# Performance work log

Measured on AMD Instinct MI355X. Metric: run time of the kernel, lower is better.

## Reference

```python
import jax, jax.numpy as jnp
import numpy as np
import math
from jax import lax

HID, H, K = 1024, 8, 4
D = HID // H
B, T = 2, 2048
CLAMP_MAX = 0.999995
LN_EPS = 1e-5

def _logit(x):
    x = min(max(x, 1e-06), 1 - 1e-06)
    return math.log(x / (1 - x))

def setup_inputs() -> dict:
    key = jax.random.key(0)
    ks = jax.random.split(key, 8)
    def xavier(k, fan_in, fan_out):
        s = math.sqrt(2.0 / (fan_in + fan_out))
        return jax.random.normal(k, (fan_in, fan_out), jnp.float32) * s
    x = jax.random.normal(ks[0], (B, T, HID), jnp.float32)
    mask = jnp.ones((B, T), jnp.float32)
    Wq = xavier(ks[1], HID, HID)
    Wk = xavier(ks[2], HID, HID)
    Wv = xavier(ks[3], HID, HID)
    Wb = xavier(ks[4], HID, H)
    bb = jnp.full((H,), _logit(0.99), jnp.float32)
    Wm = xavier(ks[5], HID, H * K)
    bm = jnp.zeros((H * K,), jnp.float32)
    Wo = xavier(ks[6], HID, HID)
    bo = jnp.zeros((HID,), jnp.float32)
    base = np.array([_logit(math.exp(-1.0 / t)) for t in [16.0, 64.0, 256.0, 1024.0]], np.float32)
    base_logit = jnp.asarray(np.tile(base[None, :], (H, 1)))  # (H, K)
    ln_g = jnp.ones((HID,), jnp.float32)
    ln_b = jnp.zeros((HID,), jnp.float32)
    return dict(x=x, mask=mask, Wq=Wq, Wk=Wk, Wv=Wv, Wb=Wb, bb=bb, Wm=Wm, bm=bm,
                Wo=Wo, bo=bo, base_logit=base_logit, ln_g=ln_g, ln_b=ln_b)

def _delta_scan(q, k, v, beta, mix, mask, base_logit):
    # q,k,v: (B,T,H,D); beta: (B,T,H); mix: (B,T,H,K); mask: (B,T)
    b, t = q.shape[0], q.shape[1]
    base_r = jax.nn.sigmoid(base_logit)  # (H,K)
    state0 = jnp.zeros((b, H, K, D, D), jnp.float32)

    def step(state, inp):
        q_t, k_t, v_t, b_t, mix_t, m_t = inp
        valid = (m_t > 0)[:, None, None, None, None]            # (B,1,1,1,1)
        r_eff = jnp.clip(b_t[:, :, None] * base_r[None], 0.0, CLAMP_MAX)  # (B,H,K)
        outer = jnp.einsum('bhd,bhe->bhde', k_t, v_t)[:, :, None]          # (B,H,1,D,D)
        new_state = jnp.where(valid, state * r_eff[..., None, None] + outer, state)
        o_scales = jnp.einsum('bhd,bhkde->bhke', q_t, new_state)           # (B,H,K,D)
        w = jax.nn.softmax(mix_t, axis=-1)                                  # (B,H,K)
        o_t = jnp.sum(w[..., None] * o_scales, axis=2)                      # (B,H,D)
        o_t = o_t * (m_t > 0)[:, None, None].astype(o_t.dtype)
        return new_state, o_t

    xs = (jnp.moveaxis(q, 1, 0), jnp.moveaxis(k, 1, 0), jnp.moveaxis(v, 1, 0),
          jnp.moveaxis(beta, 1, 0), jnp.moveaxis(mix, 1, 0), jnp.moveaxis(mask, 1, 0))
    _, outs = lax.scan(step, state0, xs)       # (T,B,H,D)
    return jnp.moveaxis(outs, 0, 1)            # (B,T,H,D)

def reference(x, mask, Wq, Wk, Wv, Wb, bb, Wm, bm, Wo, bo, base_logit, ln_g, ln_b):
    b, t, _ = x.shape
    def elu1(z):
        return jax.nn.elu(z) + 1.0
    q = elu1((x @ Wq).reshape(b, t, H, D))
    k = elu1((x @ Wk).reshape(b, t, H, D))
    v = (x @ Wv).reshape(b, t, H, D)
    beta = jax.nn.sigmoid(x @ Wb + bb)               # (B,T,H)
    mix = (x @ Wm + bm).reshape(b, t, H, K)          # (B,T,H,K)
    head_out = _delta_scan(q, k, v, beta, mix, mask, base_logit)  # (B,T,H,D)
    out = head_out.reshape(b, t, HID) @ Wo + bo
    y = x + out                                       # residual (dropout in eval mode)
    mu = jnp.mean(y, axis=-1, keepdims=True)
    var = jnp.mean((y - mu) ** 2, axis=-1, keepdims=True)
    return (y - mu) * lax.rsqrt(var + LN_EPS) * ln_g + ln_b
```

## Files before the change

### kernel.cpp

```cpp
#include <hip/hip_runtime.h>
#include <hip/hip_bf16.h>
#include <math.h>

#define TSEQ 2048
#define NHID 1024

typedef float f32x4 __attribute__((ext_vector_type(4)));
typedef __bf16 bf16x8 __attribute__((ext_vector_type(8)));

static __device__ __forceinline__ unsigned short f2bf(float f) {
  unsigned u = __float_as_uint(f);
  u += 0x7fffu + ((u >> 16) & 1u);
  return (unsigned short)(u >> 16);
}
static __device__ __forceinline__ float bf2f(unsigned short h) {
  return __uint_as_float(((unsigned)h) << 16);
}

#define GLDS16(g, l) __builtin_amdgcn_global_load_lds( \
    (const __attribute__((address_space(1))) unsigned int*)(g), \
    (__attribute__((address_space(3))) unsigned int*)(l), 16, 0, 0)

__global__ __launch_bounds__(256) void transpose_all_kernel(
    const float* __restrict__ Wq, const float* __restrict__ Wk,
    const float* __restrict__ Wv, const float* __restrict__ Wo,
    unsigned short* __restrict__ Wqkvt, unsigned short* __restrict__ Wto) {
  __shared__ float tile[32][33];
  const float* W;
  unsigned short* Wt;
  int m = blockIdx.z;
  if (m == 0)      { W = Wq; Wt = Wqkvt; }
  else if (m == 1) { W = Wk; Wt = Wqkvt + 1024 * 1024; }
  else if (m == 2) { W = Wv; Wt = Wqkvt + 2 * 1024 * 1024; }
  else             { W = Wo; Wt = Wto; }
  int bx = blockIdx.x * 32;
  int by = blockIdx.y * 32;
  int tx = threadIdx.x, ty = threadIdx.y;
#pragma unroll
  for (int i = 0; i < 32; i += 8)
    tile[ty + i][tx] = W[(size_t)(by + ty + i) * NHID + bx + tx];
  __syncthreads();
#pragma unroll
  for (int i = 0; i < 32; i += 8)
    Wt[(size_t)(bx + ty + i) * NHID + by + tx] = f2bf(tile[tx][ty + i]);
}

template <int MODE>
__global__ __launch_bounds__(256) void gemm_pipe_kernel(
    const unsigned short* __restrict__ A, const unsigned short* __restrict__ Bt,
    unsigned short* __restrict__ Oq, unsigned short* __restrict__ Ok,
    unsigned short* __restrict__ Ov, float* __restrict__ Cf,
    const float* __restrict__ bias, const float* __restrict__ res) {
  __shared__ __align__(16) unsigned short As[3 * 4096];
  __shared__ __align__(16) unsigned short Bs[3 * 4096];
  const int tid = threadIdx.x;
  const int lane = tid & 63;
  const int wave = tid >> 6;
  const int wr = wave >> 1, wc = wave & 1;
  const int rowBase = blockIdx.y * 128;
  const int colBase = blockIdx.x * 128;

  const int c0 = wave * 128 + lane;
  const int c1 = c0 + 64;
  const int r0 = c0 >> 2, kc0 = (c0 & 3) ^ ((r0 >> 1) & 3);
  const int r1 = c1 >> 2, kc1 = (c1 & 3) ^ ((r1 >> 1) & 3);
  const unsigned short* gA0 = A + (size_t)(rowBase + r0) * 1024 + kc0 * 8;
  const unsigned short* gA1 = A + (size_t)(rowBase + r1) * 1024 + kc1 * 8;
  const unsigned short* gB0 = Bt + (size_t)(colBase + r0) * 1024 + kc0 * 8;
  const unsigned short* gB1 = Bt + (size_t)(colBase + r1) * 1024 + kc1 * 8;
  const int wofs = wave * 1024;

  const int kq = lane >> 4;
  const int r16 = lane & 15;

  f32x4 acc[4][4] = {};

#define STAGE(buf, k0)                                       \
  do {                                                       \
    GLDS16(gA0 + (k0), &As[(buf) * 4096 + wofs]);            \
    GLDS16(gA1 + (k0), &As[(buf) * 4096 + wofs + 512]);      \
    GLDS16(gB0 + (k0), &Bs[(buf) * 4096 + wofs]);            \
    GLDS16(gB1 + (k0), &Bs[(buf) * 4096 + wofs + 512]);      \
  } while (0)

  STAGE(0, 0);
  STAGE(1, 32);
  int cur = 0, stg = 2;
  for (int t = 0; t < 32; ++t) {
    if (t < 30) {
      STAGE(stg, (t + 2) * 32);
      asm volatile("s_waitcnt vmcnt(8)" ::: "memory");
    } else if (t == 30) {
      asm volatile("s_waitcnt vmcnt(4)" ::: "memory");
    } else {
      asm volatile("s_waitcnt vmcnt(0)" ::: "memory");
    }
    __builtin_amdgcn_s_barrier();
    asm volatile("" ::: "memory");
    const unsigned short* Ac = &As[cur * 4096];
    const unsigned short* Bc = &Bs[cur * 4096];
    bf16x8 af[4], bfr[4];
#pragma unroll
    for (int m = 0; m < 4; ++m) {
      int row = wr * 64 + m * 16 + r16;
      af[m] = *(const bf16x8*)(Ac + row * 32 + (kq ^ ((row >> 1) & 3)) * 8);
      int colr = wc * 64 + m * 16 + r16;
      bfr[m] = *(const bf16x8*)(Bc + colr * 32 + (kq ^ ((colr >> 1) & 3)) * 8);
    }
    __builtin_amdgcn_s_setprio(1);
#pragma unroll
    for (int m = 0; m < 4; ++m)
#pragma unroll
      for (int n = 0; n < 4; ++n)
        acc[m][n] = __builtin_amdgcn_mfma_f32_16x16x32_bf16(af[m], bfr[n], acc[m][n], 0, 0, 0);
    __builtin_amdgcn_s_setprio(0);
    asm volatile("" ::: "memory");
    __builtin_amdgcn_s_barrier();
    asm volatile("" ::: "memory");
    cur = (cur == 2) ? 0 : cur + 1;
    stg = (stg == 2) ? 0 : stg + 1;
  }
#undef STAGE

  const int r4 = (lane >> 4) * 4;
  if (MODE == 1) {
#pragma unroll
    for (int m = 0; m < 4; ++m)
#pragma unroll
      for (int n = 0; n < 4; ++n) {
        int col = colBase + wc * 64 + n * 16 + r16;
#pragma unroll
        for (int j = 0; j < 4; ++j) {
          int row = rowBase + wr * 64 + m * 16 + r4 + j;
          Cf[(size_t)row * 1024 + col] = acc[m][n][j] + bias[col] + res[(size_t)row * 1024 + col];
        }
      }
  } else {
    unsigned short* outp;
    int cb;
    bool elu;
    if (colBase < 1024)      { outp = Oq; cb = colBase;        elu = true;  }
    else if (colBase < 2048) { outp = Ok; cb = colBase - 1024; elu = true;  }
    else                     { outp = Ov; cb = colBase - 2048; elu = false; }
#pragma unroll
    for (int m = 0; m < 4; ++m)
#pragma unroll
      for (int n = 0; n < 4; ++n) {
        int col = cb + wc * 64 + n * 16 + r16;
#pragma unroll
        for (int j = 0; j < 4; ++j) {
          int row = rowBase + wr * 64 + m * 16 + r4 + j;
          float v = acc[m][n][j];
          if (elu) v = (v > 0.f) ? (v + 1.f) : expf(v);
          outp[(size_t)row * 1024 + col] = f2bf(v);
        }
      }
  }
}

__global__ __launch_bounds__(256) void pack_wbm_kernel(const float* __restrict__ Wb,
    const float* __restrict__ Wm, float* __restrict__ Wt) {
  int id = blockIdx.x * 256 + threadIdx.x;
  if (id >= 40960) return;
  int o = id >> 10, i = id & 1023;
  Wt[id] = (o < 8) ? Wb[i * 8 + o] : Wm[i * 32 + (o - 8)];
}

__global__ __launch_bounds__(256) void rw2_kernel(const float* __restrict__ x,
    const float* __restrict__ Wt, const float* __restrict__ bb,
    const float* __restrict__ bm, const float* __restrict__ base_logit,
    float* __restrict__ R, float* __restrict__ Wsm,
    unsigned short* __restrict__ Xb) {
  int row = blockIdx.x;
  __shared__ float xs[1024];
  __shared__ float outs[40];
  int tid = threadIdx.x;
  float4 xv = *(const float4*)(x + (size_t)row * 1024 + tid * 4);
  *(float4*)(xs + tid * 4) = xv;
  ushort4 xo;
  xo.x = f2bf(xv.x); xo.y = f2bf(xv.y); xo.z = f2bf(xv.z); xo.w = f2bf(xv.w);
  *(ushort4*)(Xb + (size_t)row * 1024 + tid * 4) = xo;
  __syncthreads();
  int wave = tid >> 6, lane = tid & 63;
  for (int o = wave; o < 40; o += 4) {
    const float* wr = Wt + o * 1024;
    float sum = 0.f;
#pragma unroll
    for (int it = 0; it < 16; ++it) {
      int i = it * 64 + lane;
      sum += xs[i] * wr[i];
    }
#pragma unroll
    for (int off = 32; off > 0; off >>= 1) sum += __shfl_down(sum, off);
    if (lane == 0) outs[o] = sum;
  }
  __syncthreads();
  if (tid < 32) {
    int h = tid >> 2;
    float beta = 1.f / (1.f + expf(-(outs[h] + bb[h])));
    float br = 1.f / (1.f + expf(-base_logit[tid]));
    float r = fminf(fmaxf(beta * br, 0.f), 0.999995f);
    float mval = outs[8 + tid] + bm[tid];
    float mx = fmaxf(mval, __shfl_xor(mval, 1));
    mx = fmaxf(mx, __shfl_xor(mx, 2));
    float ex = expf(mval - mx);
    float ssum = ex + __shfl_xor(ex, 1);
    ssum += __shfl_xor(ssum, 2);
    R[(size_t)row * 32 + tid] = r;
    Wsm[(size_t)row * 32 + tid] = ex / ssum;
  }
}

__global__ __launch_bounds__(256) void decay2_kernel(const float* __restrict__ R,
    const float* __restrict__ Wsm, const float* __restrict__ mask,
    float* __restrict__ WA, float* __restrict__ IA, float* __restrict__ DU,
    float* __restrict__ AC) {
  int wave = threadIdx.x >> 6, lane = threadIdx.x & 63;
  int id = blockIdx.x * 4 + wave;
  int c = id & 15, k = (id >> 4) & 3, bh = id >> 6;
  int b = bh >> 3, h = bh & 7;
  int row0 = b * TSEQ + c * 128 + 2 * lane;
  float m0 = mask[row0], m1 = mask[row0 + 1];
  size_t i0 = (size_t)row0 * 32 + h * 4 + k;
  float rr0 = (m0 > 0.f) ? R[i0] : 1.f;
  float rr1 = (m1 > 0.f) ? R[i0 + 32] : 1.f;
  float incl = rr0 * rr1;
#pragma unroll
  for (int off = 1; off < 64; off <<= 1) {
    float o = __shfl_up(incl, off);
    if (lane >= off) incl *= o;
  }
  float excl = __shfl_up(incl, 1);
  if (lane == 0) excl = 1.f;
  float a0 = fmaxf(excl * rr0, 1e-25f);
  float a1 = fmaxf(a0 * rr1, 1e-25f);
  float aC = __shfl(a1, 63);
  if (lane == 63) AC[(bh * 16 + c) * 4 + k] = a1;
  bool v0 = m0 > 0.f, v1 = m1 > 0.f;
  float w0 = Wsm[i0], w1 = Wsm[i0 + 32];
  int dub = ((bh * 16 + c) * 4 + k) * 128 + 2 * lane;
  WA[i0] = v0 ? w0 * a0 : 0.f;
  WA[i0 + 32] = v1 ? w1 * a1 : 0.f;
  IA[i0] = v0 ? 1.f / a0 : 0.f;
  IA[i0 + 32] = v1 ? 1.f / a1 : 0.f;
  DU[dub] = v0 ? aC / a0 : 0.f;
  DU[dub + 1] = v1 ? aC / a1 : 0.f;
}

__global__ __launch_bounds__(512) void chunkA_kernel(
    const unsigned short* __restrict__ Qb, const unsigned short* __restrict__ Kb,
    const unsigned short* __restrict__ Vb,
    const float* __restrict__ WA, const float* __restrict__ IA,
    const float* __restrict__ DU,
    float* __restrict__ Olocal, unsigned short* __restrict__ UT) {
  __shared__ __align__(16) char KTl[32768];
  __shared__ __align__(16) char VTl[32768];
  __shared__ __align__(16) char Pl[32768];
  __shared__ __align__(16) float WAl[128][4];
  __shared__ __align__(16) float IAl[128][4];
  __shared__ float DUl[4][128];

  int wg = blockIdx.x;
  int bh = wg >> 4, c = wg & 15;
  int b = bh >> 3, h = bh & 7;
  int t0 = c * 128;
  int tid = threadIdx.x;
  int lane = tid & 63, wave = tid >> 6;
  int wbase = wave * 16;
  int l15 = lane & 15, lq = lane >> 4;

  const size_t qkvbase = ((size_t)b * TSEQ + t0) * 1024 + h * 128;

  for (int it = 0; it < 4; ++it) {
    int ci = tid + it * 512;
    int t = ci >> 4, s = ci & 15;
    bf16x8 kv = *(const bf16x8*)(Kb + qkvbase + (size_t)t * 1024 + s * 8);
    bf16x8 vv = *(const bf16x8*)(Vb + qkvbase + (size_t)t * 1024 + s * 8);
#pragma unroll
    for (int e = 0; e < 8; ++e) {
      int d = s * 8 + e;
      int off = d * 256 + (((t >> 3) ^ (d & 7)) << 4) + (t & 7) * 2;
      *(unsigned short*)(KTl + off) = f2bf((float)kv[e]);
      *(unsigned short*)(VTl + off) = f2bf((float)vv[e]);
    }
  }
  {
    int t = tid >> 2, k = tid & 3;
    size_t idx = ((size_t)b * TSEQ + t0 + t) * 32 + h * 4 + k;
    WAl[t][k] = WA[idx];
    IAl[t][k] = IA[idx];
    int k2 = tid >> 7, j = tid & 127;
    DUl[k2][j] = DU[((bh * 16 + c) * 4 + k2) * 128 + j];
  }
  __syncthreads();

  bf16x8 qf[4];
#pragma unroll
  for (int ds = 0; ds < 4; ++ds)
    qf[ds] = *(const bf16x8*)(Qb + qkvbase + (size_t)(wbase + l15) * 1024 + ds * 32 + lq * 8);
  f32x4 accP[8];
#pragma unroll
  for (int jf = 0; jf < 8; ++jf) {
    f32x4 a = {};
#pragma unroll
    for (int ds = 0; ds < 4; ++ds) {
      bf16x8 kfrag = *(const bf16x8*)(Kb + qkvbase + (size_t)(jf * 16 + l15) * 1024 + ds * 32 + lq * 8);
      a = __builtin_amdgcn_mfma_f32_16x16x32_bf16(qf[ds], kfrag, a, 0, 0, 0);
    }
    accP[jf] = a;
  }

  float4 wa4[4];
#pragma unroll
  for (int jj = 0; jj < 4; ++jj)
    wa4[jj] = *(const float4*)&WAl[wbase + lq * 4 + jj][0];
#pragma unroll
  for (int jf = 0; jf < 8; ++jf) {
    float4 ia4 = *(const float4*)&IAl[jf * 16 + l15][0];
#pragma unroll
    for (int jj = 0; jj < 4; ++jj) {
      int tl = wbase + lq * 4 + jj;
      int jl = jf * 16 + l15;
      float m = 0.f;
      if (jl <= tl)
        m = wa4[jj].x * ia4.x + wa4[jj].y * ia4.y + wa4[jj].z * ia4.z + wa4[jj].w * ia4.w;
      float pv = accP[jf][jj] * m;
      int off = tl * 256 + (((jl >> 3) ^ (tl & 7)) << 4) + (jl & 7) * 2;
      *(unsigned short*)(Pl + off) = f2bf(pv);
    }
  }

  bf16x8 pf[4];
#pragma unroll
  for (int js = 0; js < 4; ++js) {
    int tl = wbase + l15;
    int slot = js * 4 + lq;
    pf[js] = *(const bf16x8*)(Pl + tl * 256 + ((slot ^ (tl & 7)) << 4));
  }
#pragma unroll
  for (int dvf = 0; dvf < 8; ++dvf) {
    f32x4 a = {};
    int dv = dvf * 16 + l15;
#pragma unroll
    for (int js = 0; js < 4; ++js) {
      int slot = js * 4 + lq;
      bf16x8 vfrag = *(const bf16x8*)(VTl + dv * 256 + ((slot ^ (dv & 7)) << 4));
      a = __builtin_amdgcn_mfma_f32_16x16x32_bf16(pf[js], vfrag, a, 0, 0, 0);
    }
#pragma unroll
    for (int jj = 0; jj < 4; ++jj) {
      int tl = wbase + lq * 4 + jj;
      Olocal[((size_t)b * TSEQ + t0 + tl) * 1024 + h * 128 + dv] = a[jj];
    }
  }

  if (c < 15) {
#pragma unroll 1
    for (int k = 0; k < 4; ++k) {
      f32x4 accU[8] = {};
#pragma unroll 1
      for (int js = 0; js < 4; ++js) {
        int dvr = wbase + l15;
        int slot = js * 4 + lq;
        bf16x8 af = *(const bf16x8*)(VTl + dvr * 256 + ((slot ^ (dvr & 7)) << 4));
        int j0 = js * 32 + lq * 8;
        bf16x8 afs;
#pragma unroll
        for (int e = 0; e < 8; ++e)
          afs[e] = (__bf16)((float)af[e] * DUl[k][j0 + e]);
#pragma unroll
        for (int dkf = 0; dkf < 8; ++dkf) {
          int dk = dkf * 16 + l15;
          bf16x8 kf = *(const bf16x8*)(KTl + dk * 256 + ((slot ^ (dk & 7)) << 4));
          accU[dkf] = __builtin_amdgcn_mfma_f32_16x16x32_bf16(afs, kf, accU[dkf], 0, 0, 0);
        }
      }
      size_t ub = (((size_t)bh * 16 + c) * 4 + k) * 16384;
#pragma unroll
      for (int dkf = 0; dkf < 8; ++dkf) {
        int dk = dkf * 16 + l15;
#pragma unroll
        for (int jj = 0; jj < 4; ++jj) {
          int dvr = wbase + lq * 4 + jj;
          UT[ub + (size_t)dvr * 128 + dk] = f2bf(accU[dkf][jj]);
        }
      }
    }
  }
}

__global__ __launch_bounds__(256) void chainB_kernel(const unsigned short* __restrict__ UT,
    const float* __restrict__ AC, unsigned short* __restrict__ S0T) {
  int id = blockIdx.x * 256 + threadIdx.x;
  int dk = id & 127;
  int dv = (id >> 7) & 127;
  int k = (id >> 14) & 3;
  int bh = id >> 16;
  size_t elem = (size_t)dv * 128 + dk;
  float S = 0.f;
#pragma unroll 1
  for (int c = 0; c < 15; ++c) {
    size_t ub = (((size_t)bh * 16 + c) * 4 + k) * 16384;
    float u = bf2f(UT[ub + elem]);
    float aC = AC[(bh * 16 + c) * 4 + k];
    S = aC * S + u;
    size_t sb = (((size_t)bh * 16 + (c + 1)) * 4 + k) * 16384;
    S0T[sb + elem] = f2bf(S);
  }
}

__global__ __launch_bounds__(512) void chunkC_kernel(const unsigned short* __restrict__ Qb,
    const unsigned short* __restrict__ S0T, const float* __restrict__ WA,
    const float* __restrict__ Olocal, unsigned short* __restrict__ Ob) {
  __shared__ __align__(16) char Sl[32768];
  int wg = blockIdx.x;
  int bh = wg >> 4, c = wg & 15;
  int b = bh >> 3, h = bh & 7;
  int t0 = c * 128;
  int tid = threadIdx.x, lane = tid & 63, wave = tid >> 6;
  int l15 = lane & 15, lq = lane >> 4, wbase = wave * 16;
  size_t qbase = ((size_t)b * TSEQ + t0) * 1024 + h * 128;

  f32x4 accO[8] = {};
  if (c > 0) {
    int tl = wbase + l15;
#pragma unroll 1
    for (int k = 0; k < 4; ++k) {
      __syncthreads();
      size_t sb = (((size_t)bh * 16 + c) * 4 + k) * 16384;
      for (int it = 0; it < 4; ++it) {
        int ci = tid + it * 512;
        int dv = ci >> 4, s = ci & 15;
        bf16x8 vv = *(const bf16x8*)(S0T + sb + (size_t)dv * 128 + s * 8);
        *(bf16x8*)(Sl + dv * 256 + ((s ^ (dv & 7)) << 4)) = vv;
      }
      __syncthreads();
      float sc = WA[((size_t)b * TSEQ + t0 + tl) * 32 + h * 4 + k];
#pragma unroll 1
      for (int ds = 0; ds < 4; ++ds) {
        bf16x8 qf = *(const bf16x8*)(Qb + qbase + (size_t)tl * 1024 + ds * 32 + lq * 8);
        bf16x8 qs;
#pragma unroll
        for (int e = 0; e < 8; ++e) qs[e] = (__bf16)((float)qf[e] * sc);
#pragma unroll
        for (int dvf = 0; dvf < 8; ++dvf) {
          int dv = dvf * 16 + l15;
          int slot = ds * 4 + lq;
          bf16x8 sf = *(const bf16x8*)(Sl + dv * 256 + ((slot ^ (dv & 7)) << 4));
          accO[dvf] = __builtin_amdgcn_mfma_f32_16x16x32_bf16(qs, sf, accO[dvf], 0, 0, 0);
        }
      }
    }
  }
#pragma unroll
  for (int dvf = 0; dvf < 8; ++dvf) {
    int dv = dvf * 16 + l15;
#pragma unroll
    for (int jj = 0; jj < 4; ++jj) {
      int tl = wbase + lq * 4 + jj;
      size_t off = ((size_t)b * TSEQ + t0 + tl) * 1024 + h * 128 + dv;
      Ob[off] = f2bf(accO[dvf][jj] + Olocal[off]);
    }
  }
}

__global__ __launch_bounds__(256) void ln_kernel(const float* __restrict__ Y,
    const float* __restrict__ g, const float* __restrict__ bta,
    float* __restrict__ out) {
  int row = blockIdx.x;
  int tid = threadIdx.x;
  int lane = tid & 63, wave = tid >> 6;
  __shared__ float red[8];
  const float* yr = Y + (size_t)row * 1024;
  float4 v = *(const float4*)(yr + tid * 4);
  float sum = v.x + v.y + v.z + v.w;
#pragma unroll
  for (int off = 32; off > 0; off >>= 1) sum += __shfl_down(sum, off);
  if (lane == 0) red[wave] = sum;
  __syncthreads();
  float mu = (red[0] + red[1] + red[2] + red[3]) * (1.f / 1024.f);
  float4 d;
  d.x = v.x - mu; d.y = v.y - mu; d.z = v.z - mu; d.w = v.w - mu;
  float sq = d.x * d.x + d.y * d.y + d.z * d.z + d.w * d.w;
#pragma unroll
  for (int off = 32; off > 0; off >>= 1) sq += __shfl_down(sq, off);
  __syncthreads();
  if (lane == 0) red[4 + wave] = sq;
  __syncthreads();
  float var = (red[4] + red[5] + red[6] + red[7]) * (1.f / 1024.f);
  float inv = rsqrtf(var + 1e-5f);
  float4 gg = *(const float4*)(g + tid * 4);
  float4 bb4 = *(const float4*)(bta + tid * 4);
  float4 o;
  o.x = d.x * inv * gg.x + bb4.x;
  o.y = d.y * inv * gg.y + bb4.y;
  o.z = d.z * inv * gg.z + bb4.z;
  o.w = d.w * inv * gg.w + bb4.w;
  *(float4*)(out + (size_t)row * 1024 + tid * 4) = o;
}

extern "C" void kernel_launch(void* const* d_in, const int* in_sizes, int n_in,
                              void* d_out, int out_size, void* d_ws, size_t ws_size,
                              hipStream_t stream) {
  const float* x    = (const float*)d_in[0];
  const float* mask = (const float*)d_in[1];
  const float* Wq   = (const float*)d_in[2];
  const float* Wk   = (const float*)d_in[3];
  const float* Wv   = (const float*)d_in[4];
  const float* Wb   = (const float*)d_in[5];
  const float* bb   = (const float*)d_in[6];
  const float* Wm   = (const float*)d_in[7];
  const float* bm   = (const float*)d_in[8];
  const float* Wo   = (const float*)d_in[9];
  const float* bo   = (const float*)d_in[10];
  const float* base_logit = (const float*)d_in[11];
  const float* ln_g = (const float*)d_in[12];
  const float* ln_b = (const float*)d_in[13];

  char* ws = (char*)d_ws;
  const size_t MB = 1024u * 1024u;
  unsigned short* Xb    = (unsigned short*)(ws + 0);
  unsigned short* Wqkvt = (unsigned short*)(ws + 8 * MB);
  unsigned short* Wto   = (unsigned short*)(ws + 14 * MB);
  float* Rf  = (float*)(ws + 16 * MB);
  float* Wsf = (float*)(ws + 16 * MB + 512 * 1024);
  float* WAf = (float*)(ws + 17 * MB);
  float* IAf = (float*)(ws + 17 * MB + 512 * 1024);
  float* DUf = (float*)(ws + 18 * MB);
  float* ACf = (float*)(ws + 18 * MB + 512 * 1024);
  float* Wtf = (float*)(ws + 18 * MB + 768 * 1024);
  unsigned short* Qb = (unsigned short*)(ws + 19 * MB);
  unsigned short* Kb = (unsigned short*)(ws + 27 * MB);
  unsigned short* Vb = (unsigned short*)(ws + 35 * MB);
  float* Olocal = (float*)(ws + 43 * MB);
  unsigned short* Ob = (unsigned short*)(ws + 59 * MB);
  unsigned short* UTb = (unsigned short*)(ws + 67 * MB);
  unsigned short* S0T = (unsigned short*)(ws + 99 * MB);
  float* Yf = Olocal;
  if (ws_size < 131 * MB) return;

  dim3 tb(32, 8), tg(32, 32, 4);
  transpose_all_kernel<<<tg, tb, 0, stream>>>(Wq, Wk, Wv, Wo, Wqkvt, Wto);
  pack_wbm_kernel<<<160, 256, 0, stream>>>(Wb, Wm, Wtf);

  rw2_kernel<<<4096, 256, 0, stream>>>(x, Wtf, bb, bm, base_logit, Rf, Wsf, Xb);
  decay2_kernel<<<256, 256, 0, stream>>>(Rf, Wsf, mask, WAf, IAf, DUf, ACf);

  dim3 gqkv(24, 32);
  gemm_pipe_kernel<0><<<gqkv, 256, 0, stream>>>(Xb, Wqkvt, Qb, Kb, Vb, nullptr, nullptr, nullptr);

  chunkA_kernel<<<256, 512, 0, stream>>>(Qb, Kb, Vb, WAf, IAf, DUf, Olocal, UTb);
  chainB_kernel<<<4096, 256, 0, stream>>>(UTb, ACf, S0T);
  chunkC_kernel<<<256, 512, 0, stream>>>(Qb, S0T, WAf, Olocal, Ob);

  dim3 gwo(8, 32);
  gemm_pipe_kernel<1><<<gwo, 256, 0, stream>>>(Ob, Wto, nullptr, nullptr, nullptr, Yf, bo, x);

  ln_kernel<<<4096, 256, 0, stream>>>(Yf, ln_g, ln_b, (float*)d_out);
}
```

Before: 176.4 us.

## Split-K output GEMM, fold bias/residual into LN, batch rw projection rows

The output projection GEMM is split along K into two halves across blockIdx.z, doubling the grid from 256 to 512 blocks to better fill the CUs. The two partial results go to separate buffers, and the bias and residual adds move into the layernorm kernel. The small beta/mix projection kernel now handles 8 rows per block, so each weight row is loaded into registers once and reused across rows. The setprio hints around the MFMA loop are removed. The cost is extra fp32 partial-sum traffic (one more 16MB buffer written and read) and a larger shared-memory footprint in rw8.

```diff
diff --git a/kernel.cpp b/kernel.cpp
--- a/kernel.cpp
+++ b/kernel.cpp
@@ -49,8 +49,7 @@
 __global__ __launch_bounds__(256) void gemm_pipe_kernel(
     const unsigned short* __restrict__ A, const unsigned short* __restrict__ Bt,
     unsigned short* __restrict__ Oq, unsigned short* __restrict__ Ok,
-    unsigned short* __restrict__ Ov, float* __restrict__ Cf,
-    const float* __restrict__ bias, const float* __restrict__ res) {
+    unsigned short* __restrict__ Ov, float* __restrict__ P0, float* __restrict__ P1) {
   __shared__ __align__(16) unsigned short As[3 * 4096];
   __shared__ __align__(16) unsigned short Bs[3 * 4096];
   const int tid = threadIdx.x;
@@ -59,15 +58,17 @@
   const int wr = wave >> 1, wc = wave & 1;
   const int rowBase = blockIdx.y * 128;
   const int colBase = blockIdx.x * 128;
+  const int NT = (MODE == 0) ? 32 : 16;
+  const int kOff = (MODE == 0) ? 0 : blockIdx.z * 512;
 
   const int c0 = wave * 128 + lane;
   const int c1 = c0 + 64;
   const int r0 = c0 >> 2, kc0 = (c0 & 3) ^ ((r0 >> 1) & 3);
   const int r1 = c1 >> 2, kc1 = (c1 & 3) ^ ((r1 >> 1) & 3);
-  const unsigned short* gA0 = A + (size_t)(rowBase + r0) * 1024 + kc0 * 8;
-  const unsigned short* gA1 = A + (size_t)(rowBase + r1) * 1024 + kc1 * 8;
-  const unsigned short* gB0 = Bt + (size_t)(colBase + r0) * 1024 + kc0 * 8;
-  const unsigned short* gB1 = Bt + (size_t)(colBase + r1) * 1024 + kc1 * 8;
+  const unsigned short* gA0 = A + (size_t)(rowBase + r0) * 1024 + kOff + kc0 * 8;
+  const unsigned short* gA1 = A + (size_t)(rowBase + r1) * 1024 + kOff + kc1 * 8;
+  const unsigned short* gB0 = Bt + (size_t)(colBase + r0) * 1024 + kOff + kc0 * 8;
+  const unsigned short* gB1 = Bt + (size_t)(colBase + r1) * 1024 + kOff + kc1 * 8;
   const int wofs = wave * 1024;
 
   const int kq = lane >> 4;
@@ -86,11 +87,11 @@
   STAGE(0, 0);
   STAGE(1, 32);
   int cur = 0, stg = 2;
-  for (int t = 0; t < 32; ++t) {
-    if (t < 30) {
+  for (int t = 0; t < NT; ++t) {
+    if (t < NT - 2) {
       STAGE(stg, (t + 2) * 32);
       asm volatile("s_waitcnt vmcnt(8)" ::: "memory");
-    } else if (t == 30) {
+    } else if (t == NT - 2) {
       asm volatile("s_waitcnt vmcnt(4)" ::: "memory");
     } else {
       asm volatile("s_waitcnt vmcnt(0)" ::: "memory");
@@ -107,13 +108,11 @@
       int colr = wc * 64 + m * 16 + r16;
       bfr[m] = *(const bf16x8*)(Bc + colr * 32 + (kq ^ ((colr >> 1) & 3)) * 8);
     }
-    __builtin_amdgcn_s_setprio(1);
 #pragma unroll
     for (int m = 0; m < 4; ++m)
 #pragma unroll
       for (int n = 0; n < 4; ++n)
         acc[m][n] = __builtin_amdgcn_mfma_f32_16x16x32_bf16(af[m], bfr[n], acc[m][n], 0, 0, 0);
-    __builtin_amdgcn_s_setprio(0);
     asm volatile("" ::: "memory");
     __builtin_amdgcn_s_barrier();
     asm volatile("" ::: "memory");
@@ -124,6 +123,7 @@
 
   const int r4 = (lane >> 4) * 4;
   if (MODE == 1) {
+    float* P = (blockIdx.z == 0) ? P0 : P1;
 #pragma unroll
     for (int m = 0; m < 4; ++m)
 #pragma unroll
@@ -132,7 +132,7 @@
 #pragma unroll
         for (int j = 0; j < 4; ++j) {
           int row = rowBase + wr * 64 + m * 16 + r4 + j;
-          Cf[(size_t)row * 1024 + col] = acc[m][n][j] + bias[col] + res[(size_t)row * 1024 + col];
+          P[(size_t)row * 1024 + col] = acc[m][n][j];
         }
       }
   } else {
@@ -166,48 +166,56 @@
   Wt[id] = (o < 8) ? Wb[i * 8 + o] : Wm[i * 32 + (o - 8)];
 }
 
-__global__ __launch_bounds__(256) void rw2_kernel(const float* __restrict__ x,
+__global__ __launch_bounds__(256) void rw8_kernel(const float* __restrict__ x,
     const float* __restrict__ Wt, const float* __restrict__ bb,
     const float* __restrict__ bm, const float* __restrict__ base_logit,
     float* __restrict__ R, float* __restrict__ Wsm,
     unsigned short* __restrict__ Xb) {
-  int row = blockIdx.x;
-  __shared__ float xs[1024];
-  __shared__ float outs[40];
+  __shared__ float xs[8][1024];
+  __shared__ float outs[8][40];
+  int row0 = blockIdx.x * 8;
   int tid = threadIdx.x;
-  float4 xv = *(const float4*)(x + (size_t)row * 1024 + tid * 4);
-  *(float4*)(xs + tid * 4) = xv;
-  ushort4 xo;
-  xo.x = f2bf(xv.x); xo.y = f2bf(xv.y); xo.z = f2bf(xv.z); xo.w = f2bf(xv.w);
-  *(ushort4*)(Xb + (size_t)row * 1024 + tid * 4) = xo;
+#pragma unroll
+  for (int r = 0; r < 8; ++r) {
+    float4 xv = *(const float4*)(x + (size_t)(row0 + r) * 1024 + tid * 4);
+    *(float4*)(&xs[r][tid * 4]) = xv;
+    ushort4 xo;
+    xo.x = f2bf(xv.x); xo.y = f2bf(xv.y); xo.z = f2bf(xv.z); xo.w = f2bf(xv.w);
+    *(ushort4*)(Xb + (size_t)(row0 + r) * 1024 + tid * 4) = xo;
+  }
   __syncthreads();
   int wave = tid >> 6, lane = tid & 63;
   for (int o = wave; o < 40; o += 4) {
     const float* wr = Wt + o * 1024;
-    float sum = 0.f;
-#pragma unroll
-    for (int it = 0; it < 16; ++it) {
-      int i = it * 64 + lane;
-      sum += xs[i] * wr[i];
-    }
-#pragma unroll
-    for (int off = 32; off > 0; off >>= 1) sum += __shfl_down(sum, off);
-    if (lane == 0) outs[o] = sum;
-  }
-  __syncthreads();
-  if (tid < 32) {
-    int h = tid >> 2;
-    float beta = 1.f / (1.f + expf(-(outs[h] + bb[h])));
-    float br = 1.f / (1.f + expf(-base_logit[tid]));
-    float r = fminf(fmaxf(beta * br, 0.f), 0.999995f);
-    float mval = outs[8 + tid] + bm[tid];
+    float w[16];
+#pragma unroll
+    for (int it = 0; it < 16; ++it) w[it] = wr[it * 64 + lane];
+#pragma unroll
+    for (int r = 0; r < 8; ++r) {
+      float sum = 0.f;
+#pragma unroll
+      for (int it = 0; it < 16; ++it) sum += xs[r][it * 64 + lane] * w[it];
+#pragma unroll
+      for (int off = 32; off > 0; off >>= 1) sum += __shfl_down(sum, off);
+      if (lane == 0) outs[r][o] = sum;
+    }
+  }
+  __syncthreads();
+  {
+    int r = tid >> 5, j = tid & 31;
+    int row = row0 + r;
+    int h = j >> 2;
+    float beta = 1.f / (1.f + expf(-(outs[r][h] + bb[h])));
+    float br = 1.f / (1.f + expf(-base_logit[j]));
+    float rr = fminf(fmaxf(beta * br, 0.f), 0.999995f);
+    float mval = outs[r][8 + j] + bm[j];
     float mx = fmaxf(mval, __shfl_xor(mval, 1));
     mx = fmaxf(mx, __shfl_xor(mx, 2));
     float ex = expf(mval - mx);
     float ssum = ex + __shfl_xor(ex, 1);
     ssum += __shfl_xor(ssum, 2);
-    R[(size_t)row * 32 + tid] = r;
-    Wsm[(size_t)row * 32 + tid] = ex / ssum;
+    R[(size_t)row * 32 + j] = rr;
+    Wsm[(size_t)row * 32 + j] = ex / ssum;
   }
 }
 
@@ -464,15 +472,25 @@
   }
 }
 
-__global__ __launch_bounds__(256) void ln_kernel(const float* __restrict__ Y,
+__global__ __launch_bounds__(256) void ln_kernel(const float* __restrict__ P0,
+    const float* __restrict__ P1, const float* __restrict__ bo,
+    const float* __restrict__ xres,
     const float* __restrict__ g, const float* __restrict__ bta,
     float* __restrict__ out) {
   int row = blockIdx.x;
   int tid = threadIdx.x;
   int lane = tid & 63, wave = tid >> 6;
   __shared__ float red[8];
-  const float* yr = Y + (size_t)row * 1024;
-  float4 v = *(const float4*)(yr + tid * 4);
+  size_t base = (size_t)row * 1024 + tid * 4;
+  float4 a = *(const float4*)(P0 + base);
+  float4 b2 = *(const float4*)(P1 + base);
+  float4 xv = *(const float4*)(xres + base);
+  float4 bv = *(const float4*)(bo + tid * 4);
+  float4 v;
+  v.x = a.x + b2.x + bv.x + xv.x;
+  v.y = a.y + b2.y + bv.y + xv.y;
+  v.z = a.z + b2.z + bv.z + xv.z;
+  v.w = a.w + b2.w + bv.w + xv.w;
   float sum = v.x + v.y + v.z + v.w;
 #pragma unroll
   for (int off = 32; off > 0; off >>= 1) sum += __shfl_down(sum, off);
@@ -536,25 +554,26 @@
   unsigned short* Ob = (unsigned short*)(ws + 59 * MB);
   unsigned short* UTb = (unsigned short*)(ws + 67 * MB);
   unsigned short* S0T = (unsigned short*)(ws + 99 * MB);
-  float* Yf = Olocal;
+  float* Pp0 = Olocal;
+  float* Pp1 = (float*)(ws + 67 * MB);
   if (ws_size < 131 * MB) return;
 
   dim3 tb(32, 8), tg(32, 32, 4);
   transpose_all_kernel<<<tg, tb, 0, stream>>>(Wq, Wk, Wv, Wo, Wqkvt, Wto);
   pack_wbm_kernel<<<160, 256, 0, stream>>>(Wb, Wm, Wtf);
 
-  rw2_kernel<<<4096, 256, 0, stream>>>(x, Wtf, bb, bm, base_logit, Rf, Wsf, Xb);
+  rw8_kernel<<<512, 256, 0, stream>>>(x, Wtf, bb, bm, base_logit, Rf, Wsf, Xb);
   decay2_kernel<<<256, 256, 0, stream>>>(Rf, Wsf, mask, WAf, IAf, DUf, ACf);
 
   dim3 gqkv(24, 32);
-  gemm_pipe_kernel<0><<<gqkv, 256, 0, stream>>>(Xb, Wqkvt, Qb, Kb, Vb, nullptr, nullptr, nullptr);
+  gemm_pipe_kernel<0><<<gqkv, 256, 0, stream>>>(Xb, Wqkvt, Qb, Kb, Vb, nullptr, nullptr);
 
   chunkA_kernel<<<256, 512, 0, stream>>>(Qb, Kb, Vb, WAf, IAf, DUf, Olocal, UTb);
   chainB_kernel<<<4096, 256, 0, stream>>>(UTb, ACf, S0T);
   chunkC_kernel<<<256, 512, 0, stream>>>(Qb, S0T, WAf, Olocal, Ob);
 
-  dim3 gwo(8, 32);
-  gemm_pipe_kernel<1><<<gwo, 256, 0, stream>>>(Ob, Wto, nullptr, nullptr, nullptr, Yf, bo, x);
-
-  ln_kernel<<<4096, 256, 0, stream>>>(Yf, ln_g, ln_b, (float*)d_out);
-}
+  dim3 gwo(8, 32, 2);
+  gemm_pipe_kernel<1><<<gwo, 256, 0, stream>>>(Ob, Wto, nullptr, nullptr, nullptr, Pp0, Pp1);
+
+  ln_kernel<<<4096, 256, 0, stream>>>(Pp0, Pp1, bo, x, ln_g, ln_b, (float*)d_out);
+}
```

Result: no change. 175.3 us (-0.6%).
